# Kernel optimization log

Hardware: AMD Instinct MI355X
Metric: run time of the kernel (lower is better)

## Reference

```python
import jax, jax.numpy as jnp
import numpy as np

N_NODES = 100000
N_EDGES = 1200000
IN_DIM = 64
HID = 64
OUT = 10
N_GRAPHS = 256


def setup_inputs() -> dict:
    key = jax.random.key(0)
    ks = jax.random.split(key, 10)
    x = jax.random.normal(ks[0], (N_NODES, IN_DIM), dtype=jnp.float32)
    edge_index = jax.random.randint(ks[1], (2, N_EDGES), 0, N_NODES, dtype=jnp.int64)
    batch = jnp.sort(jax.random.randint(ks[2], (N_NODES,), 0, N_GRAPHS, dtype=jnp.int64))
    # GCNConv weights (glorot) and biases, final linear
    def glorot(k, fan_in, fan_out):
        s = jnp.sqrt(6.0 / (fan_in + fan_out)).astype(jnp.float32)
        return jax.random.uniform(k, (fan_in, fan_out), jnp.float32, -s, s)
    W1 = glorot(ks[3], IN_DIM, HID)
    b1 = jnp.zeros((HID,), jnp.float32)
    W2 = glorot(ks[4], HID, HID)
    b2 = jnp.zeros((HID,), jnp.float32)
    Wl = glorot(ks[5], HID, OUT)
    bl = jnp.zeros((OUT,), jnp.float32)
    return {"x": x, "edge_index": edge_index, "batch": batch,
            "W1": W1, "b1": b1, "W2": W2, "b2": b2, "Wl": Wl, "bl": bl}


def _gcn_conv(x, W, b, src, dst, n):
    # PyG GCNConv: add self-loops, symmetric deg^-1/2 normalization,
    # transform then aggregate, plus bias.
    h = x @ W  # [N, F_out]
    loop = jnp.arange(n, dtype=src.dtype)
    src_f = jnp.concatenate([src, loop])
    dst_f = jnp.concatenate([dst, loop])
    deg = jax.ops.segment_sum(jnp.ones_like(dst_f, dtype=h.dtype), dst_f, num_segments=n)
    dinv = jax.lax.rsqrt(jnp.maximum(deg, 1.0))  # self-loops guarantee deg>=1
    norm = dinv[src_f] * dinv[dst_f]  # [E+N]
    msgs = h[src_f] * norm[:, None]   # gather + scale (memory-bound)
    agg = jax.ops.segment_sum(msgs, dst_f, num_segments=n)
    return agg + b


def reference(x, edge_index, batch, W1, b1, W2, b2, Wl, bl):
    n = x.shape[0]
    src, dst = edge_index[0], edge_index[1]
    h = jax.nn.relu(_gcn_conv(x, W1, b1, src, dst, n))
    h = jax.nn.relu(_gcn_conv(h, W2, b2, src, dst, n))
    # global_mean_pool over batch vector
    sums = jax.ops.segment_sum(h, batch, num_segments=N_GRAPHS)
    cnt = jax.ops.segment_sum(jnp.ones((n,), h.dtype), batch, num_segments=N_GRAPHS)
    pooled = sums / jnp.maximum(cnt, 1.0)[:, None]  # [G, HID]
    return pooled @ Wl + bl  # [G, OUT]
```

## Files before the change

kernel.cpp:

```cpp
#include <hip/hip_runtime.h>
#include <hip/hip_bf16.h>


#define NFEAT 64
#define CAP 40

__global__ __launch_bounds__(256) void dinv_kernel(const int* __restrict__ cursor,
                                                   float* __restrict__ dinv, int n) {
    int i = blockIdx.x * blockDim.x + threadIdx.x;
    if (i < n) dinv[i] = rsqrtf((float)(cursor[i] + 1));
}

__device__ __forceinline__ void gemm_rows(const float* __restrict__ in,
                                          __hip_bfloat16* __restrict__ out,
                                          int nRows, int rowBlock,
                                          float* wl, float* xrow) {
    const int tid = threadIdx.x;
    const int lane = tid & 63;
    const int w = tid >> 6;
    const int base = rowBlock * 64 + w * 16;
    for (int i = 0; i < 16; i++) {
        int r = base + i;
        if (r >= nRows) break;
        xrow[w * 64 + lane] = in[(size_t)r * NFEAT + lane];
        float acc = 0.f;
        const float4* x4 = (const float4*)(xrow + w * 64);
        #pragma unroll
        for (int kk = 0; kk < 16; kk++) {
            float4 xv = x4[kk];
            acc = fmaf(xv.x, wl[(kk * 4 + 0) * 64 + lane], acc);
            acc = fmaf(xv.y, wl[(kk * 4 + 1) * 64 + lane], acc);
            acc = fmaf(xv.z, wl[(kk * 4 + 2) * 64 + lane], acc);
            acc = fmaf(xv.w, wl[(kk * 4 + 3) * 64 + lane], acc);
        }
        out[(size_t)r * NFEAT + lane] = __float2bfloat16(acc);
    }
}

__global__ __launch_bounds__(256) void scatter_gemm1(
        const float* __restrict__ x, const float* __restrict__ W1,
        __hip_bfloat16* __restrict__ hbuf, int nN,
        const int* __restrict__ src, const int* __restrict__ dst,
        int* __restrict__ cursor, int* __restrict__ pad, int nE, int nGemmBlk) {
    __shared__ float wl[64 * 64];
    __shared__ float xrow[4 * 64];
    const int b = blockIdx.x;
    if (b < nGemmBlk) {
        const int tid = threadIdx.x;
        #pragma unroll
        for (int i = 0; i < 16; i++) wl[tid + i * 256] = W1[tid + i * 256];
        __syncthreads();
        gemm_rows(x, hbuf, nN, b, wl, xrow);
    } else {
        int e = (b - nGemmBlk) * 256 + threadIdx.x;
        if (e < nE) {
            int d = dst[e];
            int pos = atomicAdd(&cursor[d], 1);
            if (pos < CAP) pad[(size_t)d * CAP + pos] = src[e];
        }
    }
}

__device__ __forceinline__ float agg_node(const __hip_bfloat16* __restrict__ hs,
                                          const float* __restrict__ dinv,
                                          const int* __restrict__ cursor,
                                          const int* __restrict__ pad,
                                          int n, int lane) {
    int cnt = cursor[n];
    cnt = cnt < CAP ? cnt : CAP;
    const float dn = dinv[n];
    const int* row = pad + (size_t)n * CAP;
    float acc = __bfloat162float(hs[(size_t)n * NFEAT + lane]) * dn;
    int i = 0;
    for (; i + 3 < cnt; i += 4) {
        int s0 = row[i], s1 = row[i + 1], s2 = row[i + 2], s3 = row[i + 3];
        float d0 = dinv[s0], d1 = dinv[s1], d2 = dinv[s2], d3 = dinv[s3];
        float v0 = __bfloat162float(hs[(size_t)s0 * NFEAT + lane]);
        float v1 = __bfloat162float(hs[(size_t)s1 * NFEAT + lane]);
        float v2 = __bfloat162float(hs[(size_t)s2 * NFEAT + lane]);
        float v3 = __bfloat162float(hs[(size_t)s3 * NFEAT + lane]);
        acc = fmaf(v0, d0, acc); acc = fmaf(v1, d1, acc);
        acc = fmaf(v2, d2, acc); acc = fmaf(v3, d3, acc);
    }
    for (; i < cnt; ++i) {
        int s = row[i];
        acc = fmaf(__bfloat162float(hs[(size_t)s * NFEAT + lane]), dinv[s], acc);
    }
    return acc * dn;
}

__global__ __launch_bounds__(256) void aggL1_gemm2(
        const __hip_bfloat16* __restrict__ hs1, const float* __restrict__ dinv,
        const int* __restrict__ cursor, const int* __restrict__ pad,
        const float* __restrict__ W2, const float* __restrict__ b1,
        __hip_bfloat16* __restrict__ hs2, int nN) {
    __shared__ float wl[64 * 64];
    __shared__ float xrow[4 * 64];
    const int tid = threadIdx.x;
    const int lane = tid & 63;
    const int w = tid >> 6;
    #pragma unroll
    for (int i = 0; i < 16; i++) wl[tid + i * 256] = W2[tid + i * 256];
    const float blane = b1[lane];
    __syncthreads();

    const int base = blockIdx.x * 64 + w * 16;
    for (int i = 0; i < 16; i++) {
        int n = base + i;
        if (n >= nN) break;
        float a = agg_node(hs1, dinv, cursor, pad, n, lane);
        xrow[w * 64 + lane] = fmaxf(a + blane, 0.f);
        float acc = 0.f;
        const float4* x4 = (const float4*)(xrow + w * 64);
        #pragma unroll
        for (int kk = 0; kk < 16; kk++) {
            float4 xv = x4[kk];
            acc = fmaf(xv.x, wl[(kk * 4 + 0) * 64 + lane], acc);
            acc = fmaf(xv.y, wl[(kk * 4 + 1) * 64 + lane], acc);
            acc = fmaf(xv.z, wl[(kk * 4 + 2) * 64 + lane], acc);
            acc = fmaf(xv.w, wl[(kk * 4 + 3) * 64 + lane], acc);
        }
        hs2[(size_t)n * NFEAT + lane] = __float2bfloat16(acc);
    }
}

__global__ __launch_bounds__(256) void aggL2_pool(
        const __hip_bfloat16* __restrict__ hs2, const float* __restrict__ dinv,
        const int* __restrict__ cursor, const int* __restrict__ pad,
        const float* __restrict__ b2, const int* __restrict__ batch,
        float* __restrict__ psum, int nN) {
    const int lane = threadIdx.x & 63;
    const int w = threadIdx.x >> 6;
    const int n0 = (blockIdx.x * 4 + w) * 16;
    if (n0 >= nN) return;
    const int nEnd = (n0 + 16 < nN) ? n0 + 16 : nN;
    const float b = b2[lane];
    int gprev = batch[n0];
    float pacc = 0.f;
    for (int n = n0; n < nEnd; ++n) {
        int g = batch[n];
        if (g != gprev) {
            unsafeAtomicAdd(&psum[(size_t)gprev * NFEAT + lane], pacc);
            pacc = 0.f;
            gprev = g;
        }
        float a = agg_node(hs2, dinv, cursor, pad, n, lane);
        pacc += fmaxf(a + b, 0.f);
    }
    unsafeAtomicAdd(&psum[(size_t)gprev * NFEAT + lane], pacc);
}

__global__ __launch_bounds__(64) void final_kernel(const float* __restrict__ psum,
                                                   const int* __restrict__ batch, int nN,
                                                   const float* __restrict__ Wl,
                                                   const float* __restrict__ bl,
                                                   float* __restrict__ out) {
    const int g = blockIdx.x;
    const int j = threadIdx.x;
    int lo = 0, hi = nN;
    while (lo < hi) { int mid = (lo + hi) >> 1; if (batch[mid] < g) lo = mid + 1; else hi = mid; }
    const int start = lo;
    hi = nN;
    while (lo < hi) { int mid = (lo + hi) >> 1; if (batch[mid] < g + 1) lo = mid + 1; else hi = mid; }
    const int cnt = lo - start;
    __shared__ float p[64];
    p[j] = psum[g * 64 + j] / (float)(cnt > 1 ? cnt : 1);
    __syncthreads();
    if (j < 10) {
        float acc = bl[j];
        #pragma unroll
        for (int f = 0; f < 64; f++) acc = fmaf(p[f], Wl[f * 10 + j], acc);
        out[g * 10 + j] = acc;
    }
}

static inline size_t align256(size_t s) { return (s + 255) & ~(size_t)255; }

extern "C" void kernel_launch(void* const* d_in, const int* in_sizes, int n_in,
                              void* d_out, int out_size, void* d_ws, size_t ws_size,
                              hipStream_t stream) {
    const float* x     = (const float*)d_in[0];
    const int*   ei    = (const int*)d_in[1];
    const int*   batch = (const int*)d_in[2];
    const float* W1    = (const float*)d_in[3];
    const float* b1    = (const float*)d_in[4];
    const float* W2    = (const float*)d_in[5];
    const float* b2    = (const float*)d_in[6];
    const float* Wl    = (const float*)d_in[7];
    const float* bl    = (const float*)d_in[8];
    float* out = (float*)d_out;

    const int nN = in_sizes[0] / NFEAT;
    const int nE = in_sizes[1] / 2;
    const int nG = 256;
    const int* src = ei;
    const int* dst = ei + nE;

    char* w = (char*)d_ws;
    float* dinv   = (float*)w; w += align256((size_t)nN * 4);
    int*   cursor = (int*)w;   w += align256((size_t)nN * 4);
    int*   pad    = (int*)w;   w += align256((size_t)nN * CAP * 4);
    __hip_bfloat16* hs1 = (__hip_bfloat16*)w; w += align256((size_t)nN * NFEAT * 2);
    __hip_bfloat16* hs2 = (__hip_bfloat16*)w; w += align256((size_t)nN * NFEAT * 2);
    float* psum   = (float*)w; w += align256((size_t)nG * NFEAT * 4);

    const int nBlkN   = (nN + 255) / 256;
    const int nBlkE   = (nE + 255) / 256;
    const int nBlkRow = (nN + 63) / 64;

    hipMemsetAsync(cursor, 0, (size_t)nN * 4, stream);
    hipMemsetAsync(psum, 0, (size_t)nG * NFEAT * 4, stream);

    scatter_gemm1<<<nBlkRow + nBlkE, 256, 0, stream>>>(
        x, W1, hs1, nN, src, dst, cursor, pad, nE, nBlkRow);
    dinv_kernel<<<nBlkN, 256, 0, stream>>>(cursor, dinv, nN);

    aggL1_gemm2<<<nBlkRow, 256, 0, stream>>>(hs1, dinv, cursor, pad, W2, b1, hs2, nN);

    aggL2_pool<<<nBlkRow, 256, 0, stream>>>(hs2, dinv, cursor, pad, b2, batch, psum, nN);

    final_kernel<<<nG, 64, 0, stream>>>(psum, batch, nN, Wl, bl, out);
}
```

Baseline: 244.7 us.

## Partition edge scatter by XCD destination range and compute dinv on the fly

The edge scatter now runs on persistent blocks. Each block reads its XCD id and only handles destinations in that XCD's node range, so atomics on cursor and writes to the padded adjacency stay in one XCD's L2. Blocks take edge chunks from a per-XCD atomic counter, and every XCD reads all edges. The separate dinv kernel is removed: degrees are turned into rsqrt inline from cursor inside aggregation, which adds rsqrt work and int loads in place of float loads. The two memsets become one contiguous memset. Correctness depends on blocks being spread across all 8 XCDs; if some XCD gets no scatter blocks, its destination range is never processed.

```diff
diff --git a/kernel.cpp b/kernel.cpp
--- a/kernel.cpp
+++ b/kernel.cpp
@@ -4,12 +4,7 @@
 
 #define NFEAT 64
 #define CAP 40
-
-__global__ __launch_bounds__(256) void dinv_kernel(const int* __restrict__ cursor,
-                                                   float* __restrict__ dinv, int n) {
-    int i = blockIdx.x * blockDim.x + threadIdx.x;
-    if (i < n) dinv[i] = rsqrtf((float)(cursor[i] + 1));
-}
+#define CHUNK_E 2048
 
 __device__ __forceinline__ void gemm_rows(const float* __restrict__ in,
                                           __hip_bfloat16* __restrict__ out,
@@ -41,40 +36,59 @@
         const float* __restrict__ x, const float* __restrict__ W1,
         __hip_bfloat16* __restrict__ hbuf, int nN,
         const int* __restrict__ src, const int* __restrict__ dst,
-        int* __restrict__ cursor, int* __restrict__ pad, int nE, int nGemmBlk) {
+        int* __restrict__ cursor, int* __restrict__ xcdCnt,
+        int* __restrict__ pad, int nE,
+        int nScatBlk, int nChunks, int rng) {
     __shared__ float wl[64 * 64];
     __shared__ float xrow[4 * 64];
     const int b = blockIdx.x;
-    if (b < nGemmBlk) {
+    if (b >= nScatBlk) {
         const int tid = threadIdx.x;
         #pragma unroll
         for (int i = 0; i < 16; i++) wl[tid + i * 256] = W1[tid + i * 256];
         __syncthreads();
-        gemm_rows(x, hbuf, nN, b, wl, xrow);
+        gemm_rows(x, hbuf, nN, b - nScatBlk, wl, xrow);
     } else {
-        int e = (b - nGemmBlk) * 256 + threadIdx.x;
-        if (e < nE) {
-            int d = dst[e];
-            int pos = atomicAdd(&cursor[d], 1);
-            if (pos < CAP) pad[(size_t)d * CAP + pos] = src[e];
+        int xcd;
+        asm volatile("s_getreg_b32 %0, hwreg(HW_REG_XCC_ID)" : "=s"(xcd));
+        xcd &= 7;
+        const int lo = xcd * rng;
+        __shared__ int sChunk;
+        for (;;) {
+            __syncthreads();
+            if (threadIdx.x == 0) sChunk = atomicAdd(&xcdCnt[xcd], 1);
+            __syncthreads();
+            const int chunk = sChunk;
+            if (chunk >= nChunks) break;
+            int e0 = chunk * CHUNK_E;
+            int e1 = e0 + CHUNK_E; if (e1 > nE) e1 = nE;
+            for (int e = e0 + threadIdx.x; e < e1; e += 256) {
+                int d = dst[e];
+                if ((unsigned)(d - lo) < (unsigned)rng) {
+                    int pos = atomicAdd(&cursor[d], 1);
+                    if (pos < CAP) pad[(size_t)d * CAP + pos] = src[e];
+                }
+            }
         }
     }
 }
 
 __device__ __forceinline__ float agg_node(const __hip_bfloat16* __restrict__ hs,
-                                          const float* __restrict__ dinv,
                                           const int* __restrict__ cursor,
                                           const int* __restrict__ pad,
                                           int n, int lane) {
-    int cnt = cursor[n];
-    cnt = cnt < CAP ? cnt : CAP;
-    const float dn = dinv[n];
+    const int deg = cursor[n];
+    const int cnt = deg < CAP ? deg : CAP;
+    const float dn = rsqrtf((float)(deg + 1));
     const int* row = pad + (size_t)n * CAP;
     float acc = __bfloat162float(hs[(size_t)n * NFEAT + lane]) * dn;
     int i = 0;
     for (; i + 3 < cnt; i += 4) {
         int s0 = row[i], s1 = row[i + 1], s2 = row[i + 2], s3 = row[i + 3];
-        float d0 = dinv[s0], d1 = dinv[s1], d2 = dinv[s2], d3 = dinv[s3];
+        float d0 = rsqrtf((float)(cursor[s0] + 1));
+        float d1 = rsqrtf((float)(cursor[s1] + 1));
+        float d2 = rsqrtf((float)(cursor[s2] + 1));
+        float d3 = rsqrtf((float)(cursor[s3] + 1));
         float v0 = __bfloat162float(hs[(size_t)s0 * NFEAT + lane]);
         float v1 = __bfloat162float(hs[(size_t)s1 * NFEAT + lane]);
         float v2 = __bfloat162float(hs[(size_t)s2 * NFEAT + lane]);
@@ -84,13 +98,14 @@
     }
     for (; i < cnt; ++i) {
         int s = row[i];
-        acc = fmaf(__bfloat162float(hs[(size_t)s * NFEAT + lane]), dinv[s], acc);
+        acc = fmaf(__bfloat162float(hs[(size_t)s * NFEAT + lane]),
+                   rsqrtf((float)(cursor[s] + 1)), acc);
     }
     return acc * dn;
 }
 
 __global__ __launch_bounds__(256) void aggL1_gemm2(
-        const __hip_bfloat16* __restrict__ hs1, const float* __restrict__ dinv,
+        const __hip_bfloat16* __restrict__ hs1,
         const int* __restrict__ cursor, const int* __restrict__ pad,
         const float* __restrict__ W2, const float* __restrict__ b1,
         __hip_bfloat16* __restrict__ hs2, int nN) {
@@ -108,7 +123,7 @@
     for (int i = 0; i < 16; i++) {
         int n = base + i;
         if (n >= nN) break;
-        float a = agg_node(hs1, dinv, cursor, pad, n, lane);
+        float a = agg_node(hs1, cursor, pad, n, lane);
         xrow[w * 64 + lane] = fmaxf(a + blane, 0.f);
         float acc = 0.f;
         const float4* x4 = (const float4*)(xrow + w * 64);
@@ -125,7 +140,7 @@
 }
 
 __global__ __launch_bounds__(256) void aggL2_pool(
-        const __hip_bfloat16* __restrict__ hs2, const float* __restrict__ dinv,
+        const __hip_bfloat16* __restrict__ hs2,
         const int* __restrict__ cursor, const int* __restrict__ pad,
         const float* __restrict__ b2, const int* __restrict__ batch,
         float* __restrict__ psum, int nN) {
@@ -144,7 +159,7 @@
             pacc = 0.f;
             gprev = g;
         }
-        float a = agg_node(hs2, dinv, cursor, pad, n, lane);
+        float a = agg_node(hs2, cursor, pad, n, lane);
         pacc += fmaxf(a + b, 0.f);
     }
     unsafeAtomicAdd(&psum[(size_t)gprev * NFEAT + lane], pacc);
@@ -197,27 +212,28 @@
     const int* dst = ei + nE;
 
     char* w = (char*)d_ws;
-    float* dinv   = (float*)w; w += align256((size_t)nN * 4);
-    int*   cursor = (int*)w;   w += align256((size_t)nN * 4);
+    int*   cursor = (int*)w;
+    int*   xcdCnt = cursor + nN;
+    float* psum   = (float*)(xcdCnt + 8);
+    const size_t zeroBytes = ((size_t)nN + 8 + (size_t)nG * NFEAT) * 4;
+    w += align256(zeroBytes);
     int*   pad    = (int*)w;   w += align256((size_t)nN * CAP * 4);
     __hip_bfloat16* hs1 = (__hip_bfloat16*)w; w += align256((size_t)nN * NFEAT * 2);
     __hip_bfloat16* hs2 = (__hip_bfloat16*)w; w += align256((size_t)nN * NFEAT * 2);
-    float* psum   = (float*)w; w += align256((size_t)nG * NFEAT * 4);
-
-    const int nBlkN   = (nN + 255) / 256;
-    const int nBlkE   = (nE + 255) / 256;
-    const int nBlkRow = (nN + 63) / 64;
-
-    hipMemsetAsync(cursor, 0, (size_t)nN * 4, stream);
-    hipMemsetAsync(psum, 0, (size_t)nG * NFEAT * 4, stream);
-
-    scatter_gemm1<<<nBlkRow + nBlkE, 256, 0, stream>>>(
-        x, W1, hs1, nN, src, dst, cursor, pad, nE, nBlkRow);
-    dinv_kernel<<<nBlkN, 256, 0, stream>>>(cursor, dinv, nN);
-
-    aggL1_gemm2<<<nBlkRow, 256, 0, stream>>>(hs1, dinv, cursor, pad, W2, b1, hs2, nN);
-
-    aggL2_pool<<<nBlkRow, 256, 0, stream>>>(hs2, dinv, cursor, pad, b2, batch, psum, nN);
+
+    const int nBlkRow  = (nN + 63) / 64;
+    const int nScatBlk = 2048;
+    const int nChunks  = (nE + CHUNK_E - 1) / CHUNK_E;
+    const int rng      = (nN + 7) / 8;
+
+    hipMemsetAsync(cursor, 0, zeroBytes, stream);
+
+    scatter_gemm1<<<nScatBlk + nBlkRow, 256, 0, stream>>>(
+        x, W1, hs1, nN, src, dst, cursor, xcdCnt, pad, nE, nScatBlk, nChunks, rng);
+
+    aggL1_gemm2<<<nBlkRow, 256, 0, stream>>>(hs1, cursor, pad, W2, b1, hs2, nN);
+
+    aggL2_pool<<<nBlkRow, 256, 0, stream>>>(hs2, cursor, pad, b2, batch, psum, nN);
 
     final_kernel<<<nG, 64, 0, stream>>>(psum, batch, nN, Wl, bl, out);
 }
```

After: 302.8 us. +23.7%, slower.
